# Optimization experiments

Measured on AMD Instinct MI355X. Metric: run time of the kernel, lower is better.

## Reference

```python
import jax, jax.numpy as jnp
import numpy as np
import math

GROUPS = 32
EPS = 1e-5
NUM_HEADS = 8


def group_norm(x, gamma, beta):
    # x: [B, C, H, W]; normalize within each of GROUPS channel groups over (C/G, H, W)
    B, C, H, W = x.shape
    xg = x.reshape(B, GROUPS, C // GROUPS, H, W)
    mean = jnp.mean(xg, axis=(2, 3, 4), keepdims=True)
    var = jnp.var(xg, axis=(2, 3, 4), keepdims=True)
    xn = ((xg - mean) * jax.lax.rsqrt(var + EPS)).reshape(B, C, H, W)
    return xn * gamma[None, :, None, None] + beta[None, :, None, None]


def setup_inputs() -> dict:
    key = jax.random.key(0)
    ks = jax.random.split(key, 10)
    C = 512
    B, H, W = 2, 64, 64
    s = 1.0 / math.sqrt(C)
    return {
        "x": jax.random.normal(ks[0], (B, C, H, W), jnp.float32),
        "gamma": jnp.ones((C,), jnp.float32),
        "beta": jnp.zeros((C,), jnp.float32),
        "Wq": jax.random.normal(ks[1], (C, C), jnp.float32) * s,
        "bq": jax.random.normal(ks[2], (C,), jnp.float32) * 0.01,
        "Wk": jax.random.normal(ks[3], (C, C), jnp.float32) * s,
        "bk": jax.random.normal(ks[4], (C,), jnp.float32) * 0.01,
        "Wv": jax.random.normal(ks[5], (C, C), jnp.float32) * s,
        "bv": jax.random.normal(ks[6], (C,), jnp.float32) * 0.01,
        "Wo": jax.random.normal(ks[7], (C, C), jnp.float32) * s,
        "bo": jax.random.normal(ks[8], (C,), jnp.float32) * 0.01,
    }


def reference(x, gamma, beta, Wq, bq, Wk, bk, Wv, bv, Wo, bo):
    B, C, H, W = x.shape
    N = H * W
    hd = C // NUM_HEADS
    h = group_norm(x, gamma, beta)
    h = h.reshape(B, C, N).transpose(0, 2, 1)  # [B, N, C]
    # torch nn.Linear: y = x @ W.T + b
    q = (h @ Wq.T + bq).reshape(B, N, NUM_HEADS, hd)
    k = (h @ Wk.T + bk).reshape(B, N, NUM_HEADS, hd)
    v = (h @ Wv.T + bv).reshape(B, N, NUM_HEADS, hd)
    scale = 1.0 / math.sqrt(hd)
    attn = jnp.einsum('bihd,bjhd->bijh', q, k) * scale  # [B, N, N, heads]
    attn = jax.nn.softmax(attn, axis=2)
    o = jnp.einsum('bijh,bjhd->bihd', attn, v).reshape(B, N, C)
    o = o @ Wo.T + bo
    o = o.transpose(0, 2, 1).reshape(B, C, H, W)
    return x + o
```

## Files before the change

kernel.cpp:

```cpp
#include <hip/hip_runtime.h>
#include <cstdint>
#include <cstddef>

typedef __bf16 bf16x8 __attribute__((ext_vector_type(8)));
typedef float f32x4 __attribute__((ext_vector_type(4)));
typedef float f32x16 __attribute__((ext_vector_type(16)));
typedef unsigned short ushort8 __attribute__((ext_vector_type(8)));
typedef unsigned u32x2 __attribute__((ext_vector_type(2)));
typedef float f4 __attribute__((ext_vector_type(4)));

__device__ __forceinline__ unsigned short f2bf(float f) {
    __bf16 b = (__bf16)f;
    return *(unsigned short*)&b;
}
__device__ __forceinline__ unsigned pk2bf(float a, float b) {
    __bf16 x = (__bf16)a, y = (__bf16)b;
    unsigned short ux = *(unsigned short*)&x, uy = *(unsigned short*)&y;
    return (unsigned)ux | ((unsigned)uy << 16);
}
__device__ __forceinline__ float bf2f(unsigned short u) {
    union { unsigned u; float f; } v; v.u = ((unsigned)u) << 16; return v.f;
}

#if __has_builtin(__builtin_amdgcn_exp2f)
#define EXP2(x) __builtin_amdgcn_exp2f(x)
#else
#define EXP2(x) exp2f(x)
#endif

__device__ __forceinline__ void pl32swap(unsigned& x, unsigned& y) {
#if __has_builtin(__builtin_amdgcn_permlane32_swap)
    auto r = __builtin_amdgcn_permlane32_swap(x, y, false, false);
    x = r[0]; y = r[1];
#else
    unsigned xs = (unsigned)__shfl_xor((int)x, 32, 64);
    unsigned ys = (unsigned)__shfl_xor((int)y, 32, 64);
    bool lo = ((threadIdx.x & 63) < 32);
    unsigned nx = lo ? x : ys;
    unsigned ny = lo ? xs : y;
    x = nx; y = ny;
#endif
}

#define GLL(g, l) __builtin_amdgcn_global_load_lds( \
    (__attribute__((address_space(1))) void*)(g), \
    (__attribute__((address_space(3))) void*)(l), 16, 0, 0)

#define CS 0.18033688011112042f
#define SPLITS 2

__global__ __launch_bounds__(256) void prep(
    const float* __restrict__ wq, const float* __restrict__ wk,
    const float* __restrict__ wv, const float* __restrict__ wo,
    unsigned short* __restrict__ wb,
    const float* __restrict__ x, float* __restrict__ part)
{
    const int bid = blockIdx.x;
    if (bid < 4096) {
        int i = bid * 256 + threadIdx.x;
        const float* src = (i < 262144) ? wq : (i < 524288) ? wk : (i < 786432) ? wv : wo;
        wb[i] = f2bf(src[i & 262143]);
        return;
    }
    const int blk = bid - 4096;
    const int q = blk & 3, bg = blk >> 2;
    const f4* xv = (const f4*)(x + (size_t)bg * 65536 + q * 16384);
    float s = 0.f, sq = 0.f;
    for (int i = threadIdx.x; i < 4096; i += 256) {
        f4 v = xv[i];
        s  += v.x + v.y + v.z + v.w;
        sq += v.x * v.x + v.y * v.y + v.z * v.z + v.w * v.w;
    }
    #pragma unroll
    for (int off = 32; off > 0; off >>= 1) {
        s  += __shfl_xor(s, off, 64);
        sq += __shfl_xor(sq, off, 64);
    }
    __shared__ float red[8];
    const int w = threadIdx.x >> 6, lane = threadIdx.x & 63;
    if (lane == 0) { red[w] = s; red[4 + w] = sq; }
    __syncthreads();
    if (threadIdx.x == 0) {
        part[(bg * 4 + q) * 2]     = red[0] + red[1] + red[2] + red[3];
        part[(bg * 4 + q) * 2 + 1] = red[4] + red[5] + red[6] + red[7];
    }
}

__global__ __launch_bounds__(256) void gn_apply(
    const float* __restrict__ x, const float* __restrict__ gamma,
    const float* __restrict__ beta, const float* __restrict__ part,
    unsigned short* __restrict__ h)
{
    const int q = blockIdx.x, bg = blockIdx.y;
    const int b = bg >> 5, g = bg & 31;
    float s = 0.f, sq = 0.f;
    #pragma unroll
    for (int j = 0; j < 4; ++j) {
        s  += part[(bg * 4 + j) * 2];
        sq += part[(bg * 4 + j) * 2 + 1];
    }
    const float mean = s * (1.f / 65536.f);
    const float rstd = rsqrtf(sq * (1.f / 65536.f) - mean * mean + 1e-5f);

    float gm[16], bt[16];
    #pragma unroll
    for (int c = 0; c < 16; ++c) {
        gm[c] = gamma[g * 16 + c] * rstd;
        bt[c] = beta[g * 16 + c];
    }
    const float* xg = x + (size_t)bg * 65536;
    const int n0 = q * 1024 + threadIdx.x * 4;
    float val[16][4];
    #pragma unroll
    for (int c = 0; c < 16; ++c) {
        f4 v = *(const f4*)&xg[(size_t)c * 4096 + n0];
        val[c][0] = (v.x - mean) * gm[c] + bt[c];
        val[c][1] = (v.y - mean) * gm[c] + bt[c];
        val[c][2] = (v.z - mean) * gm[c] + bt[c];
        val[c][3] = (v.w - mean) * gm[c] + bt[c];
    }
    #pragma unroll
    for (int nn = 0; nn < 4; ++nn) {
        ushort8 v0, v1;
        #pragma unroll
        for (int c = 0; c < 8; ++c)  v0[c]     = f2bf(val[c][nn]);
        #pragma unroll
        for (int c = 8; c < 16; ++c) v1[c - 8] = f2bf(val[c][nn]);
        unsigned short* dst = h + ((size_t)(b * 4096 + n0 + nn)) * 512 + g * 16;
        *(ushort8*)dst = v0;
        *(ushort8*)(dst + 8) = v1;
    }
}

__global__ __launch_bounds__(256, 2) void gemm_qkv(
    const unsigned short* __restrict__ A,
    const unsigned short* __restrict__ Bt,
    const float* __restrict__ bias0,
    const float* __restrict__ bias1,
    const float* __restrict__ bias2,
    unsigned short* __restrict__ outB,
    unsigned short* __restrict__ vtout,
    int M, int N, int K)
{
    __shared__ __attribute__((aligned(16))) unsigned short As[128 * 32];
    __shared__ __attribute__((aligned(16))) unsigned short Bs[128 * 32];
    const int t = threadIdx.x;
    const int w = t >> 6, lane = t & 63;
    const int l15 = lane & 15, l4 = lane >> 4;
    const int bm = blockIdx.y, bn = blockIdx.x;
    const int wm = (w >> 1) * 64, wn = (w & 1) * 64;

    f32x4 acc[4][4] = {};

    const int srow = t >> 2;
    const int sc8  = (t & 3) * 8;

    const unsigned short* gA0 = A  + (size_t)(bm * 128 + srow) * K + sc8;
    const unsigned short* gA1 = gA0 + (size_t)64 * K;
    const unsigned short* gB0 = Bt + (size_t)(bn * 128 + srow) * K + sc8;
    const unsigned short* gB1 = gB0 + (size_t)64 * K;
    unsigned short* lA0 = &As[w * 512];
    unsigned short* lA1 = &As[2048 + w * 512];
    unsigned short* lB0 = &Bs[w * 512];
    unsigned short* lB1 = &Bs[2048 + w * 512];

    for (int k0 = 0; k0 < K; k0 += 32) {
        __syncthreads();
        GLL(gA0 + k0, lA0);
        GLL(gA1 + k0, lA1);
        GLL(gB0 + k0, lB0);
        GLL(gB1 + k0, lB1);
        __syncthreads();

        bf16x8 af[4], bfr[4];
        #pragma unroll
        for (int mt = 0; mt < 4; ++mt)
            af[mt] = *(const bf16x8*)&As[(wm + mt * 16 + l15) * 32 + l4 * 8];
        #pragma unroll
        for (int nt = 0; nt < 4; ++nt)
            bfr[nt] = *(const bf16x8*)&Bs[(wn + nt * 16 + l15) * 32 + l4 * 8];
        #pragma unroll
        for (int mt = 0; mt < 4; ++mt)
            #pragma unroll
            for (int nt = 0; nt < 4; ++nt)
                acc[mt][nt] = __builtin_amdgcn_mfma_f32_16x16x32_bf16(
                    af[mt], bfr[nt], acc[mt][nt], 0, 0, 0);
    }

    #pragma unroll
    for (int nt = 0; nt < 4; ++nt) {
        int col = bn * 128 + wn + nt * 16 + l15;
        const float* bp = (col < 512) ? bias0 : (col < 1024) ? bias1 : bias2;
        float bv = bp[col & 511];
        if (col < 1024) {
            float sc = (col < 512) ? CS : 1.0f;
            #pragma unroll
            for (int mt = 0; mt < 4; ++mt)
                #pragma unroll
                for (int r = 0; r < 4; ++r) {
                    int row = bm * 128 + wm + mt * 16 + l4 * 4 + r;
                    outB[(size_t)row * 1024 + col] = f2bf((acc[mt][nt][r] + bv) * sc);
                }
        } else {
            int hd = col - 1024;
            #pragma unroll
            for (int mt = 0; mt < 4; ++mt) {
                int m = bm * 128 + wm + mt * 16 + l4 * 4;
                int bb = m >> 12, n = m & 4095;
                unsigned u0 = pk2bf(acc[mt][nt][0] + bv, acc[mt][nt][1] + bv);
                unsigned u1 = pk2bf(acc[mt][nt][2] + bv, acc[mt][nt][3] + bv);
                unsigned short* dst = vtout +
                    ((size_t)(bb * 8 + (hd >> 6)) * 64 + (hd & 63)) * 4096 + n;
                *(u32x2*)dst = (u32x2){u0, u1};
            }
        }
    }
}

__global__ __launch_bounds__(512, 2) void gemm_out(
    const unsigned short* __restrict__ A,
    const unsigned short* __restrict__ Bt,
    const float* __restrict__ bias,
    const float* __restrict__ resid,
    float* __restrict__ outF)
{
    __shared__ __attribute__((aligned(16))) unsigned short As[128 * 32];
    __shared__ __attribute__((aligned(16))) unsigned short Bs[128 * 32];
    const int t = threadIdx.x;
    const int w = t >> 6, lane = t & 63;
    const int l15 = lane & 15, l4 = lane >> 4;
    const int bm = blockIdx.y, bn = blockIdx.x;
    const int wm = (w >> 2) * 64, wn = (w & 3) * 32;

    f32x4 acc[4][2] = {};

    const int srow = t >> 2, sc8 = (t & 3) * 8;
    const unsigned short* gA = A  + (size_t)(bm * 128 + srow) * 512 + sc8;
    const unsigned short* gB = Bt + (size_t)(bn * 128 + srow) * 512 + sc8;
    unsigned short* lA = &As[t * 8];
    unsigned short* lB = &Bs[t * 8];

    for (int k0 = 0; k0 < 512; k0 += 32) {
        __syncthreads();
        GLL(gA + k0, lA);
        GLL(gB + k0, lB);
        __syncthreads();

        bf16x8 af[4], bfr[2];
        #pragma unroll
        for (int mt = 0; mt < 4; ++mt)
            af[mt] = *(const bf16x8*)&As[(wm + mt * 16 + l15) * 32 + l4 * 8];
        #pragma unroll
        for (int nt = 0; nt < 2; ++nt)
            bfr[nt] = *(const bf16x8*)&Bs[(wn + nt * 16 + l15) * 32 + l4 * 8];
        #pragma unroll
        for (int mt = 0; mt < 4; ++mt)
            #pragma unroll
            for (int nt = 0; nt < 2; ++nt)
                acc[mt][nt] = __builtin_amdgcn_mfma_f32_16x16x32_bf16(
                    af[mt], bfr[nt], acc[mt][nt], 0, 0, 0);
    }

    #pragma unroll
    for (int mt = 0; mt < 4; ++mt)
        #pragma unroll
        for (int nt = 0; nt < 2; ++nt)
            #pragma unroll
            for (int r = 0; r < 4; ++r) {
                int c = bm * 128 + wm + mt * 16 + l4 * 4 + r;
                int m = bn * 128 + wn + nt * 16 + l15;
                int b = m >> 12, n = m & 4095;
                size_t idx = ((size_t)(b * 512 + c)) * 4096 + n;
                outF[idx] = acc[mt][nt][r] + bias[c] + resid[idx];
            }
}

__global__ __launch_bounds__(256, 2) void attn_kernel(
    const unsigned short* __restrict__ qkv, const unsigned short* __restrict__ vt,
    unsigned short* __restrict__ opart, float* __restrict__ lbuf)
{
    __shared__ __attribute__((aligned(16))) unsigned short Sh[2 * 64 * 72];
    unsigned short* KsB  = Sh;
    unsigned short* VtsB = Sh + 64 * 72;

    const int bh = blockIdx.y, b = bh >> 3, h = bh & 7;
    const int qbase = blockIdx.x * 256;
    const int s = blockIdx.z, ks0 = s * 2048;
    const int t = threadIdx.x, w = t >> 6, lane = t & 63;
    const int l31 = lane & 31, h5 = lane >> 5;

    const unsigned short* Qg = qkv + ((size_t)(b * 4096 + qbase + w * 64)) * 1024 + h * 64;
    const unsigned short* Kg = qkv + ((size_t)(b * 4096 + ks0)) * 1024 + 512 + h * 64;
    const unsigned short* Vg = vt + ((size_t)bh) * 64 * 4096 + ks0;

    bf16x8 qf[2][4];
    #pragma unroll
    for (int qt = 0; qt < 2; ++qt)
        #pragma unroll
        for (int kc = 0; kc < 4; ++kc)
            qf[qt][kc] = *(const bf16x8*)(Qg + (size_t)(qt * 32 + l31) * 1024 + kc * 16 + h5 * 8);

    f32x16 Oacc[2][2] = {};
    float li[2] = {0.f, 0.f};

    const int sr = t >> 2, sc = (t & 3) * 16;
    const unsigned short* gK = Kg + (size_t)sr * 1024 + sc;
    const unsigned short* gV = Vg + (size_t)sr * 4096 + sc;
    unsigned short* lK = KsB + sr * 72 + sc;
    unsigned short* lV = VtsB + sr * 72 + sc;

    ushort8 kr[2], vr[2];
    kr[0] = *(const ushort8*)(gK);
    kr[1] = *(const ushort8*)(gK + 8);
    vr[0] = *(const ushort8*)(gV);
    vr[1] = *(const ushort8*)(gV + 8);

    for (int kt = 0; kt < 32; ++kt) {
        __syncthreads();
        *(ushort8*)(lK)     = kr[0];
        *(ushort8*)(lK + 8) = kr[1];
        *(ushort8*)(lV)     = vr[0];
        *(ushort8*)(lV + 8) = vr[1];
        __syncthreads();
        if (kt < 31) {
            const unsigned short* nk = gK + (size_t)(kt + 1) * 65536;
            const unsigned short* nv = gV + (kt + 1) * 64;
            kr[0] = *(const ushort8*)(nk);
            kr[1] = *(const ushort8*)(nk + 8);
            vr[0] = *(const ushort8*)(nv);
            vr[1] = *(const ushort8*)(nv + 8);
        }

        f32x16 St[2][2] = {};
        #pragma unroll
        for (int ct = 0; ct < 2; ++ct)
            #pragma unroll
            for (int kc = 0; kc < 4; ++kc) {
                bf16x8 kf = *(const bf16x8*)(KsB + (ct * 32 + l31) * 72 + kc * 16 + h5 * 8);
                St[0][ct] = __builtin_amdgcn_mfma_f32_32x32x16_bf16(kf, qf[0][kc], St[0][ct], 0, 0, 0);
                St[1][ct] = __builtin_amdgcn_mfma_f32_32x32x16_bf16(kf, qf[1][kc], St[1][ct], 0, 0, 0);
            }

        union PU { unsigned u[4]; bf16x8 v; };
        PU pf[2][4];
        #pragma unroll
        for (int qt = 0; qt < 2; ++qt) {
            #pragma unroll
            for (int ct = 0; ct < 2; ++ct)
                #pragma unroll
                for (int r = 0; r < 16; ++r)
                    St[qt][ct][r] = EXP2(St[qt][ct][r]);
            float s0 = 0.f, s1 = 0.f;
            #pragma unroll
            for (int ct = 0; ct < 2; ++ct) {
                s0 += ((St[qt][ct][0] + St[qt][ct][1]) + (St[qt][ct][2] + St[qt][ct][3]))
                    + ((St[qt][ct][4] + St[qt][ct][5]) + (St[qt][ct][6] + St[qt][ct][7]));
                s1 += ((St[qt][ct][8] + St[qt][ct][9]) + (St[qt][ct][10] + St[qt][ct][11]))
                    + ((St[qt][ct][12] + St[qt][ct][13]) + (St[qt][ct][14] + St[qt][ct][15]));
            }
            li[qt] += s0 + s1;

            #pragma unroll
            for (int ct = 0; ct < 2; ++ct) {
                unsigned pk0 = pk2bf(St[qt][ct][0],  St[qt][ct][1]);
                unsigned pk1 = pk2bf(St[qt][ct][2],  St[qt][ct][3]);
                unsigned pk2 = pk2bf(St[qt][ct][4],  St[qt][ct][5]);
                unsigned pk3 = pk2bf(St[qt][ct][6],  St[qt][ct][7]);
                unsigned pk4 = pk2bf(St[qt][ct][8],  St[qt][ct][9]);
                unsigned pk5 = pk2bf(St[qt][ct][10], St[qt][ct][11]);
                unsigned pk6 = pk2bf(St[qt][ct][12], St[qt][ct][13]);
                unsigned pk7 = pk2bf(St[qt][ct][14], St[qt][ct][15]);
                pl32swap(pk0, pk2); pl32swap(pk1, pk3);
                pl32swap(pk4, pk6); pl32swap(pk5, pk7);
                pf[qt][ct * 2].u[0] = pk0; pf[qt][ct * 2].u[1] = pk1;
                pf[qt][ct * 2].u[2] = pk2; pf[qt][ct * 2].u[3] = pk3;
                pf[qt][ct * 2 + 1].u[0] = pk4; pf[qt][ct * 2 + 1].u[1] = pk5;
                pf[qt][ct * 2 + 1].u[2] = pk6; pf[qt][ct * 2 + 1].u[3] = pk7;
            }
        }

        #pragma unroll
        for (int kk = 0; kk < 4; ++kk)
            #pragma unroll
            for (int dt = 0; dt < 2; ++dt) {
                bf16x8 vf = *(const bf16x8*)(VtsB + (dt * 32 + l31) * 72 + kk * 16 + h5 * 8);
                Oacc[dt][0] = __builtin_amdgcn_mfma_f32_32x32x16_bf16(vf, pf[0][kk].v, Oacc[dt][0], 0, 0, 0);
                Oacc[dt][1] = __builtin_amdgcn_mfma_f32_32x32x16_bf16(vf, pf[1][kk].v, Oacc[dt][1], 0, 0, 0);
            }
    }

    #pragma unroll
    for (int qt = 0; qt < 2; ++qt) {
        float lf = li[qt] + __shfl_xor(li[qt], 32, 64);
        if (h5 == 0)
            lbuf[((size_t)s * 16 + bh) * 4096 + qbase + w * 64 + qt * 32 + l31] = lf;
    }

    __syncthreads();
    unsigned short* Eb = Sh + w * (32 * 72);
    #pragma unroll
    for (int qt = 0; qt < 2; ++qt) {
        #pragma unroll
        for (int dt = 0; dt < 2; ++dt)
            #pragma unroll
            for (int p = 0; p < 8; ++p) {
                int d = dt * 32 + 2 * (p & 1) + 8 * (p >> 1) + 4 * h5;
                unsigned u = pk2bf(Oacc[dt][qt][2 * p], Oacc[dt][qt][2 * p + 1]);
                *(unsigned*)&Eb[l31 * 72 + d] = u;
            }
        unsigned short* Og = opart +
            (((size_t)s * 16 + bh) * 4096 + qbase + w * 64 + qt * 32) * 64;
        #pragma unroll
        for (int i = 0; i < 4; ++i) {
            int c8 = h5 * 4 + i;
            ushort8 val = *(const ushort8*)&Eb[l31 * 72 + c8 * 8];
            *(ushort8*)(Og + (size_t)l31 * 64 + c8 * 8) = val;
        }
    }
}

__global__ __launch_bounds__(256) void combine_o(
    const unsigned short* __restrict__ opart, const float* __restrict__ lbuf,
    unsigned short* __restrict__ o)
{
    int gid = blockIdx.x * 256 + threadIdx.x;
    int row = gid >> 3, c8 = gid & 7;
    int bh = row >> 12, q = row & 4095;
    int b = bh >> 3, h = bh & 7;
    float l = 0.f;
    #pragma unroll
    for (int sp = 0; sp < SPLITS; ++sp)
        l += lbuf[(size_t)sp * 65536 + row];
    float inv = 1.f / l;
    float acc[8] = {};
    #pragma unroll
    for (int sp = 0; sp < SPLITS; ++sp) {
        ushort8 ov = *(const ushort8*)(opart +
            (size_t)sp * 65536 * 64 + (size_t)row * 64 + c8 * 8);
        #pragma unroll
        for (int i = 0; i < 8; ++i) acc[i] += bf2f(ov[i]);
    }
    ushort8 r;
    #pragma unroll
    for (int i = 0; i < 8; ++i) r[i] = f2bf(acc[i] * inv);
    *(ushort8*)(o + ((size_t)(b * 4096 + q)) * 512 + h * 64 + c8 * 8) = r;
}

extern "C" void kernel_launch(void* const* d_in, const int* in_sizes, int n_in,
                              void* d_out, int out_size, void* d_ws, size_t ws_size,
                              hipStream_t stream) {
    const float* x     = (const float*)d_in[0];
    const float* gamma = (const float*)d_in[1];
    const float* beta  = (const float*)d_in[2];
    const float* Wq    = (const float*)d_in[3];
    const float* bq    = (const float*)d_in[4];
    const float* Wk    = (const float*)d_in[5];
    const float* bk    = (const float*)d_in[6];
    const float* Wv    = (const float*)d_in[7];
    const float* bv    = (const float*)d_in[8];
    const float* Wo    = (const float*)d_in[9];
    const float* bo    = (const float*)d_in[10];
    float* out = (float*)d_out;

    char* ws = (char*)d_ws;
    const size_t MB = 1024 * 1024;
    unsigned short* wb     = (unsigned short*)(ws);
    float*          gnpart = (float*)(ws + 2 * MB);
    unsigned short* qkv    = (unsigned short*)(ws + 3 * MB);
    unsigned short* vtb    = (unsigned short*)(ws + 19 * MB);
    unsigned short* h      = (unsigned short*)(ws + 27 * MB);
    unsigned short* opart  = (unsigned short*)(ws + 27 * MB);
    float*          lbuf   = (float*)(ws + 59 * MB);
    unsigned short* obuf   = qkv;

    prep<<<dim3(4352), dim3(256), 0, stream>>>(Wq, Wk, Wv, Wo, wb, x, gnpart);
    gn_apply<<<dim3(4, 64), dim3(256), 0, stream>>>(x, gamma, beta, gnpart, h);

    gemm_qkv<<<dim3(12, 64), dim3(256), 0, stream>>>(
        h, wb, bq, bk, bv, qkv, vtb, 8192, 1536, 512);

    attn_kernel<<<dim3(16, 16, SPLITS), dim3(256), 0, stream>>>(qkv, vtb, opart, lbuf);
    combine_o<<<dim3(2048), dim3(256), 0, stream>>>(opart, lbuf, obuf);

    gemm_out<<<dim3(64, 4), dim3(512), 0, stream>>>(
        wb + 786432, obuf, bo, x, out);
}
```

Before: 219.1 us.

## Fuse split-attention combine into output GEMM and use 512-thread QKV GEMM

```diff
diff --git a/kernel.cpp b/kernel.cpp
--- a/kernel.cpp
+++ b/kernel.cpp
@@ -132,15 +132,14 @@
     }
 }
 
-__global__ __launch_bounds__(256, 2) void gemm_qkv(
+__global__ __launch_bounds__(512, 2) void gemm_qkv(
     const unsigned short* __restrict__ A,
     const unsigned short* __restrict__ Bt,
     const float* __restrict__ bias0,
     const float* __restrict__ bias1,
     const float* __restrict__ bias2,
     unsigned short* __restrict__ outB,
-    unsigned short* __restrict__ vtout,
-    int M, int N, int K)
+    unsigned short* __restrict__ vtout)
 {
     __shared__ __attribute__((aligned(16))) unsigned short As[128 * 32];
     __shared__ __attribute__((aligned(16))) unsigned short Bs[128 * 32];
@@ -148,47 +147,39 @@
     const int w = t >> 6, lane = t & 63;
     const int l15 = lane & 15, l4 = lane >> 4;
     const int bm = blockIdx.y, bn = blockIdx.x;
-    const int wm = (w >> 1) * 64, wn = (w & 1) * 64;
-
-    f32x4 acc[4][4] = {};
-
-    const int srow = t >> 2;
-    const int sc8  = (t & 3) * 8;
-
-    const unsigned short* gA0 = A  + (size_t)(bm * 128 + srow) * K + sc8;
-    const unsigned short* gA1 = gA0 + (size_t)64 * K;
-    const unsigned short* gB0 = Bt + (size_t)(bn * 128 + srow) * K + sc8;
-    const unsigned short* gB1 = gB0 + (size_t)64 * K;
-    unsigned short* lA0 = &As[w * 512];
-    unsigned short* lA1 = &As[2048 + w * 512];
-    unsigned short* lB0 = &Bs[w * 512];
-    unsigned short* lB1 = &Bs[2048 + w * 512];
-
-    for (int k0 = 0; k0 < K; k0 += 32) {
-        __syncthreads();
-        GLL(gA0 + k0, lA0);
-        GLL(gA1 + k0, lA1);
-        GLL(gB0 + k0, lB0);
-        GLL(gB1 + k0, lB1);
-        __syncthreads();
-
-        bf16x8 af[4], bfr[4];
+    const int wm = (w >> 2) * 64, wn = (w & 3) * 32;
+
+    f32x4 acc[4][2] = {};
+
+    const int srow = t >> 2, sc8 = (t & 3) * 8;
+    const unsigned short* gA = A  + (size_t)(bm * 128 + srow) * 512 + sc8;
+    const unsigned short* gB = Bt + (size_t)(bn * 128 + srow) * 512 + sc8;
+    unsigned short* lA = &As[t * 8];
+    unsigned short* lB = &Bs[t * 8];
+
+    for (int k0 = 0; k0 < 512; k0 += 32) {
+        __syncthreads();
+        GLL(gA + k0, lA);
+        GLL(gB + k0, lB);
+        __syncthreads();
+
+        bf16x8 af[4], bfr[2];
         #pragma unroll
         for (int mt = 0; mt < 4; ++mt)
             af[mt] = *(const bf16x8*)&As[(wm + mt * 16 + l15) * 32 + l4 * 8];
         #pragma unroll
-        for (int nt = 0; nt < 4; ++nt)
+        for (int nt = 0; nt < 2; ++nt)
             bfr[nt] = *(const bf16x8*)&Bs[(wn + nt * 16 + l15) * 32 + l4 * 8];
         #pragma unroll
         for (int mt = 0; mt < 4; ++mt)
             #pragma unroll
-            for (int nt = 0; nt < 4; ++nt)
+            for (int nt = 0; nt < 2; ++nt)
                 acc[mt][nt] = __builtin_amdgcn_mfma_f32_16x16x32_bf16(
                     af[mt], bfr[nt], acc[mt][nt], 0, 0, 0);
     }
 
     #pragma unroll
-    for (int nt = 0; nt < 4; ++nt) {
+    for (int nt = 0; nt < 2; ++nt) {
         int col = bn * 128 + wn + nt * 16 + l15;
         const float* bp = (col < 512) ? bias0 : (col < 1024) ? bias1 : bias2;
         float bv = bp[col & 511];
@@ -219,7 +210,8 @@
 
 __global__ __launch_bounds__(512, 2) void gemm_out(
     const unsigned short* __restrict__ A,
-    const unsigned short* __restrict__ Bt,
+    const unsigned short* __restrict__ opart,
+    const float* __restrict__ lbuf,
     const float* __restrict__ bias,
     const float* __restrict__ resid,
     float* __restrict__ outF)
@@ -235,15 +227,39 @@
     f32x4 acc[4][2] = {};
 
     const int srow = t >> 2, sc8 = (t & 3) * 8;
-    const unsigned short* gA = A  + (size_t)(bm * 128 + srow) * 512 + sc8;
-    const unsigned short* gB = Bt + (size_t)(bn * 128 + srow) * 512 + sc8;
+    const unsigned short* gA = A + (size_t)(bm * 128 + srow) * 512 + sc8;
     unsigned short* lA = &As[t * 8];
     unsigned short* lB = &Bs[t * 8];
 
+    const int m = bn * 128 + srow;
+    const int bb = m >> 12, q = m & 4095;
+    const size_t prow0 = (size_t)(bb * 8) * 4096 + q;
+    float inv[8];
+    #pragma unroll
+    for (int hh = 0; hh < 8; ++hh) {
+        size_t pr = prow0 + (size_t)hh * 4096;
+        inv[hh] = 1.f / (lbuf[pr] + lbuf[65536 + pr]);
+    }
+    const unsigned short* gO0 = opart + prow0 * 64;
+    const unsigned short* gO1 = gO0 + (size_t)65536 * 64;
+
+    ushort8 o0 = *(const ushort8*)(gO0 + sc8);
+    ushort8 o1 = *(const ushort8*)(gO1 + sc8);
+
     for (int k0 = 0; k0 < 512; k0 += 32) {
+        float iv = inv[k0 >> 6];
+        ushort8 bv8;
+        #pragma unroll
+        for (int i = 0; i < 8; ++i)
+            bv8[i] = f2bf((bf2f(o0[i]) + bf2f(o1[i])) * iv);
+        if (k0 < 480) {
+            size_t noff = (size_t)((k0 + 32) >> 6) * 262144 + ((k0 + 32) & 32) + sc8;
+            o0 = *(const ushort8*)(gO0 + noff);
+            o1 = *(const ushort8*)(gO1 + noff);
+        }
         __syncthreads();
         GLL(gA + k0, lA);
-        GLL(gB + k0, lB);
+        *(ushort8*)lB = bv8;
         __syncthreads();
 
         bf16x8 af[4], bfr[2];
@@ -268,8 +284,8 @@
             #pragma unroll
             for (int r = 0; r < 4; ++r) {
                 int c = bm * 128 + wm + mt * 16 + l4 * 4 + r;
-                int m = bn * 128 + wn + nt * 16 + l15;
-                int b = m >> 12, n = m & 4095;
+                int mm = bn * 128 + wn + nt * 16 + l15;
+                int b = mm >> 12, n = mm & 4095;
                 size_t idx = ((size_t)(b * 512 + c)) * 4096 + n;
                 outF[idx] = acc[mt][nt][r] + bias[c] + resid[idx];
             }
@@ -419,33 +435,6 @@
     }
 }
 
-__global__ __launch_bounds__(256) void combine_o(
-    const unsigned short* __restrict__ opart, const float* __restrict__ lbuf,
-    unsigned short* __restrict__ o)
-{
-    int gid = blockIdx.x * 256 + threadIdx.x;
-    int row = gid >> 3, c8 = gid & 7;
-    int bh = row >> 12, q = row & 4095;
-    int b = bh >> 3, h = bh & 7;
-    float l = 0.f;
-    #pragma unroll
-    for (int sp = 0; sp < SPLITS; ++sp)
-        l += lbuf[(size_t)sp * 65536 + row];
-    float inv = 1.f / l;
-    float acc[8] = {};
-    #pragma unroll
-    for (int sp = 0; sp < SPLITS; ++sp) {
-        ushort8 ov = *(const ushort8*)(opart +
-            (size_t)sp * 65536 * 64 + (size_t)row * 64 + c8 * 8);
-        #pragma unroll
-        for (int i = 0; i < 8; ++i) acc[i] += bf2f(ov[i]);
-    }
-    ushort8 r;
-    #pragma unroll
-    for (int i = 0; i < 8; ++i) r[i] = f2bf(acc[i] * inv);
-    *(ushort8*)(o + ((size_t)(b * 4096 + q)) * 512 + h * 64 + c8 * 8) = r;
-}
-
 extern "C" void kernel_launch(void* const* d_in, const int* in_sizes, int n_in,
                               void* d_out, int out_size, void* d_ws, size_t ws_size,
                               hipStream_t stream) {
@@ -471,17 +460,15 @@
     unsigned short* h      = (unsigned short*)(ws + 27 * MB);
     unsigned short* opart  = (unsigned short*)(ws + 27 * MB);
     float*          lbuf   = (float*)(ws + 59 * MB);
-    unsigned short* obuf   = qkv;
 
     prep<<<dim3(4352), dim3(256), 0, stream>>>(Wq, Wk, Wv, Wo, wb, x, gnpart);
     gn_apply<<<dim3(4, 64), dim3(256), 0, stream>>>(x, gamma, beta, gnpart, h);
 
-    gemm_qkv<<<dim3(12, 64), dim3(256), 0, stream>>>(
-        h, wb, bq, bk, bv, qkv, vtb, 8192, 1536, 512);
+    gemm_qkv<<<dim3(12, 64), dim3(512), 0, stream>>>(
+        h, wb, bq, bk, bv, qkv, vtb);
 
     attn_kernel<<<dim3(16, 16, SPLITS), dim3(256), 0, stream>>>(qkv, vtb, opart, lbuf);
-    combine_o<<<dim3(2048), dim3(256), 0, stream>>>(opart, lbuf, obuf);
 
     gemm_out<<<dim3(64, 4), dim3(512), 0, stream>>>(
-        wb + 786432, obuf, bo, x, out);
-}
+        wb + 786432, opart, lbuf, bo, x, out);
+}
```

After: 219.4 us. Within noise of the previous version (+0.1%).
